# Kernel optimization log

Measured on AMD Instinct MI355X. Metric: run time of the kernel, lower is better.

The kernel has to match this reference:

```python
import jax, jax.numpy as jnp
import numpy as np

EPS_NORM = 1e-12   # torch F.normalize eps
EPS_COND = 1e-10   # conductance denominator eps (matches source)


def _metrics(rep, b):
    # rep: (N, D) float, b: (N,) int 0/1 boundaries
    N = rep.shape[0]
    S = rep @ rep.T                                   # (N, N) similarity
    # F.normalize(sim, p=2, dim=-1): L2-normalize each row
    S = S / jnp.maximum(jnp.linalg.norm(S, axis=-1, keepdims=True), EPS_NORM)
    comm = jnp.cumsum(b)                              # (N,) community ids in [0, N]
    total = S.sum()
    deg = S.sum(axis=1)                               # row sums
    # modularity: sum over same-community (i, j) of S_ij - deg_i*deg_j/total, then /total
    same = comm[:, None] == comm[None, :]
    mod = jnp.sum(jnp.where(same, S - deg[:, None] * deg[None, :] / total, 0.0)) / total
    # conductance via segment sums over community ids (num_segments fixed = N+1)
    C = N + 1
    A = jax.ops.segment_sum(S, comm, num_segments=C)          # (C, N): sum over rows i in comm c
    B2 = jax.ops.segment_sum(A.T, comm, num_segments=C)      # (C_j, C_i)
    within = jnp.diagonal(B2)                                 # within-community edge weight
    row_tot = A.sum(axis=1)                                   # total weight incident to comm c
    between = row_tot - within
    counts = jax.ops.segment_sum(jnp.ones((N,), dtype=S.dtype), comm, num_segments=C)
    nonempty = counts > 0
    cond_terms = jnp.where(nonempty, between / (2.0 * within + between + EPS_COND), 0.0)
    n_comms = jnp.maximum(nonempty.sum(), 1).astype(S.dtype)
    cond = cond_terms.sum() / n_comms
    return mod, cond


def setup_inputs() -> dict:
    key = jax.random.key(0)
    k1, k2 = jax.random.split(key)
    representations = jax.random.normal(k1, (8, 2048, 512), dtype=jnp.float32)
    boundaries = jax.random.randint(k2, (8, 2048), 0, 2, dtype=jnp.int32)
    return {"representations": representations, "boundaries": boundaries}


def reference(representations, boundaries):
    mod, cond = jax.vmap(_metrics)(representations, boundaries)
    # (2, B): row 0 = modularity per batch, row 1 = conductance per batch
    return jnp.stack([mod, cond], axis=0)
```

## Files before the change

kernel.cpp:

```cpp
#include <hip/hip_runtime.h>
#include <hip/hip_bf16.h>

constexpr int BATCH = 8;
constexpr int N = 2048;
constexpr int D = 512;

using short8 = __attribute__((ext_vector_type(8))) short;
using half8 = __attribute__((ext_vector_type(8))) _Float16;
using floatx4 = __attribute__((ext_vector_type(4))) float;

__global__ __launch_bounds__(256) void convert_kernel(const float* __restrict__ in,
                                                      unsigned short* __restrict__ hi,
                                                      unsigned short* __restrict__ lo) {
    size_t base = ((size_t)blockIdx.x * 256 + threadIdx.x) * 8;
    float v[8];
    *(float4*)(v) = *(const float4*)(in + base);
    *(float4*)(v + 4) = *(const float4*)(in + base + 4);
    short8 h, l;
#pragma unroll
    for (int e = 0; e < 8; ++e) {
        _Float16 hh = (_Float16)v[e];
        float r = v[e] - (float)hh;
        _Float16 ll = (_Float16)r;
        h[e] = __builtin_bit_cast(short, hh);
        l[e] = __builtin_bit_cast(short, ll);
    }
    *(short8*)(hi + base) = h;
    *(short8*)(lo + base) = l;
}

__global__ __launch_bounds__(256) void scan_kernel(const int* __restrict__ b,
                                                   int* __restrict__ comm,
                                                   float* __restrict__ stats ) {
    int batch = blockIdx.x;
    int t = threadIdx.x;

    {
        int idx = batch * 256 + t;
        float* p = stats;
#pragma unroll
        for (int u = 0; u < 24; ++u) p[idx + u * 2048] = 0.0f;
    }

    const int* bb = b + batch * N;
    int* cc = comm + batch * N;

    int vals[8];
    int s = 0;
#pragma unroll
    for (int u = 0; u < 8; ++u) { vals[u] = bb[t * 8 + u]; s += vals[u]; }

    __shared__ int ps[256];
    ps[t] = s;
    __syncthreads();
    for (int off = 1; off < 256; off <<= 1) {
        int v = (t >= off) ? ps[t - off] : 0;
        __syncthreads();
        ps[t] += v;
        __syncthreads();
    }
    int run = (t > 0) ? ps[t - 1] : 0;
#pragma unroll
    for (int u = 0; u < 8; ++u) { run += vals[u]; cc[t * 8 + u] = run; }
}

__global__ __launch_bounds__(256, 3) void gemm_mfma(
        const unsigned short* __restrict__ Hhi, const unsigned short* __restrict__ Hlo,
        const int* __restrict__ comm,
        float* __restrict__ ssq, float* __restrict__ sm, float* __restrict__ bs) {
    int batch = blockIdx.z;

    int t = blockIdx.x;
    int bi = 0;
    while (t >= (16 - bi)) { t -= (16 - bi); ++bi; }
    int bj = bi + t;
    bool diag = (bi == bj);
    int i0 = bi * 128, j0 = bj * 128;

    __shared__ unsigned short sAhi[4096], sAlo[4096], sBhi[4096], sBlo[4096];
    __shared__ int sci[128], scj[128];

    int tid = threadIdx.x;
    const int* cm = comm + batch * N;
    if (tid < 128) { sci[tid] = cm[i0 + tid]; scj[tid] = cm[j0 + tid]; }

    const size_t bo = (size_t)batch * N * D;
    int srow = tid >> 2;
    int kg = (tid & 3) ^ ((srow >> 1) & 3);
    size_t gA0 = bo + (size_t)(i0 + srow) * D + kg * 8;
    size_t gA1 = gA0 + (size_t)64 * D;
    size_t gB0 = bo + (size_t)(j0 + srow) * D + kg * 8;
    size_t gB1 = gB0 + (size_t)64 * D;

    int lane = tid & 63;
    int wv = tid >> 6;
    int wrow = wv >> 1, wcol = wv & 1;
    int l15 = lane & 15, lhi = lane >> 4;

    int offA[4], offB[4];
#pragma unroll
    for (int m = 0; m < 4; ++m) {
        int r = wrow * 64 + m * 16 + l15;
        offA[m] = r * 64 + ((lhi ^ ((r >> 1) & 3)) << 4);
        int c = wcol * 64 + m * 16 + l15;
        offB[m] = c * 64 + ((lhi ^ ((c >> 1) & 3)) << 4);
    }

    floatx4 acc[4][4];
#pragma unroll
    for (int m = 0; m < 4; ++m)
#pragma unroll
        for (int n = 0; n < 4; ++n) acc[m][n] = (floatx4){0.f, 0.f, 0.f, 0.f};

    int wbyte = tid * 16;

    short8 rAh0 = *(const short8*)(Hhi + gA0);
    short8 rAh1 = *(const short8*)(Hhi + gA1);
    short8 rAl0 = *(const short8*)(Hlo + gA0);
    short8 rAl1 = *(const short8*)(Hlo + gA1);
    short8 rBh0 = *(const short8*)(Hhi + gB0);
    short8 rBh1 = *(const short8*)(Hhi + gB1);
    short8 rBl0 = *(const short8*)(Hlo + gB0);
    short8 rBl1 = *(const short8*)(Hlo + gB1);

#pragma unroll 1
    for (int kt = 0; kt < 16; ++kt) {
        *(short8*)((char*)sAhi + wbyte) = rAh0;
        *(short8*)((char*)sAhi + wbyte + 4096) = rAh1;
        *(short8*)((char*)sAlo + wbyte) = rAl0;
        *(short8*)((char*)sAlo + wbyte + 4096) = rAl1;
        *(short8*)((char*)sBhi + wbyte) = rBh0;
        *(short8*)((char*)sBhi + wbyte + 4096) = rBh1;
        *(short8*)((char*)sBlo + wbyte) = rBl0;
        *(short8*)((char*)sBlo + wbyte + 4096) = rBl1;
        __syncthreads();

        if (kt < 15) {
            size_t k = (size_t)(kt + 1) * 32;
            rAh0 = *(const short8*)(Hhi + gA0 + k);
            rAh1 = *(const short8*)(Hhi + gA1 + k);
            rAl0 = *(const short8*)(Hlo + gA0 + k);
            rAl1 = *(const short8*)(Hlo + gA1 + k);
            rBh0 = *(const short8*)(Hhi + gB0 + k);
            rBh1 = *(const short8*)(Hhi + gB1 + k);
            rBl0 = *(const short8*)(Hlo + gB0 + k);
            rBl1 = *(const short8*)(Hlo + gB1 + k);
        }

        half8 ah[4], al[4], bh[4], bl[4];
#pragma unroll
        for (int m = 0; m < 4; ++m) {
            ah[m] = *(const half8*)((const char*)sAhi + offA[m]);
            al[m] = *(const half8*)((const char*)sAlo + offA[m]);
            bh[m] = *(const half8*)((const char*)sBhi + offB[m]);
            bl[m] = *(const half8*)((const char*)sBlo + offB[m]);
        }
#pragma unroll
        for (int m = 0; m < 4; ++m)
#pragma unroll
            for (int n = 0; n < 4; ++n) {
                acc[m][n] = __builtin_amdgcn_mfma_f32_16x16x32_f16(ah[m], bh[n], acc[m][n], 0, 0, 0);
                acc[m][n] = __builtin_amdgcn_mfma_f32_16x16x32_f16(ah[m], bl[n], acc[m][n], 0, 0, 0);
                acc[m][n] = __builtin_amdgcn_mfma_f32_16x16x32_f16(al[m], bh[n], acc[m][n], 0, 0, 0);
            }
        __syncthreads();
    }

    float* pssq = ssq + batch * N;
    float* psm = sm + batch * N;
    float* pbs = bs + batch * N;

    int cjv[4];
#pragma unroll
    for (int n = 0; n < 4; ++n) cjv[n] = scj[wcol * 64 + n * 16 + l15];

    float cq[4] = {0.f, 0.f, 0.f, 0.f};
    float cs[4] = {0.f, 0.f, 0.f, 0.f};
    float cb[4] = {0.f, 0.f, 0.f, 0.f};

#pragma unroll
    for (int m = 0; m < 4; ++m) {
#pragma unroll
        for (int rr = 0; rr < 4; ++rr) {
            int rloc = wrow * 64 + m * 16 + lhi * 4 + rr;
            int civ = sci[rloc];
            float vq = 0.f, vs = 0.f, vb = 0.f;
#pragma unroll
            for (int n = 0; n < 4; ++n) {
                float g = acc[m][n][rr];
                float gq = g * g;
                float gb = (civ == cjv[n]) ? g : 0.f;
                vq += gq; vs += g; vb += gb;
                cq[n] += gq; cs[n] += g; cb[n] += gb;
            }
#pragma unroll
            for (int msk = 8; msk >= 1; msk >>= 1) {
                vq += __shfl_xor(vq, msk);
                vs += __shfl_xor(vs, msk);
                vb += __shfl_xor(vb, msk);
            }
            if (l15 == 0) {
                atomicAdd(&pssq[i0 + rloc], vq);
                atomicAdd(&psm[i0 + rloc], vs);
                atomicAdd(&pbs[i0 + rloc], vb);
            }
        }
    }

    if (!diag) {
#pragma unroll
        for (int n = 0; n < 4; ++n) {
            cq[n] += __shfl_xor(cq[n], 16); cq[n] += __shfl_xor(cq[n], 32);
            cs[n] += __shfl_xor(cs[n], 16); cs[n] += __shfl_xor(cs[n], 32);
            cb[n] += __shfl_xor(cb[n], 16); cb[n] += __shfl_xor(cb[n], 32);
            if (lhi == 0) {
                int col = j0 + wcol * 64 + n * 16 + l15;
                atomicAdd(&pssq[col], cq[n]);
                atomicAdd(&psm[col], cs[n]);
                atomicAdd(&pbs[col], cb[n]);
            }
        }
    }
}

__global__ __launch_bounds__(1024) void finalize(const float* __restrict__ ssq,
                                                 const float* __restrict__ sm,
                                                 const float* __restrict__ bs,
                                                 const int* __restrict__ comm,
                                                 float* __restrict__ out) {
    int batch = blockIdx.x;
    const float* pssq = ssq + batch * N;
    const float* psm = sm + batch * N;
    const float* pbs = bs + batch * N;
    const int* pcomm = comm + batch * N;
    int tid = threadIdx.x;

    __shared__ float sWc[N + 1];
    __shared__ float sTc[N + 1];
    __shared__ int sCnt[N + 1];

    for (int c = tid; c < N + 1; c += 1024) { sWc[c] = 0.0f; sTc[c] = 0.0f; sCnt[c] = 0; }
    __syncthreads();

    float totalLocal = 0.0f;
    for (int i = tid; i < N; i += 1024) {
        float r = sqrtf(pssq[i]);
        r = fmaxf(r, 1e-12f);
        float deg = psm[i] / r;
        float bn = pbs[i] / r;
        int c = pcomm[i];
        atomicAdd(&sTc[c], deg);
        atomicAdd(&sWc[c], bn);
        atomicAdd(&sCnt[c], 1);
        totalLocal += deg;
    }
    __syncthreads();

    float sumW = 0.0f, sumT2 = 0.0f, condSum = 0.0f, ncomm = 0.0f;
    for (int c = tid; c < N + 1; c += 1024) {
        if (sCnt[c] > 0) {
            float W = sWc[c];
            float T = sTc[c];
            sumW += W;
            sumT2 += T * T;
            float between = T - W;
            condSum += between / (2.0f * W + between + 1e-10f);
            ncomm += 1.0f;
        }
    }

    float vals[5] = {totalLocal, sumW, sumT2, condSum, ncomm};
#pragma unroll
    for (int v = 0; v < 5; ++v)
#pragma unroll
        for (int m = 32; m >= 1; m >>= 1) vals[v] += __shfl_xor(vals[v], m);

    __shared__ float part[5][16];
    int wid = tid >> 6;
    if ((tid & 63) == 0) {
#pragma unroll
        for (int v = 0; v < 5; ++v) part[v][wid] = vals[v];
    }
    __syncthreads();

    if (tid == 0) {
        float red[5];
#pragma unroll
        for (int v = 0; v < 5; ++v) {
            float a = 0.f;
            for (int w = 0; w < 16; ++w) a += part[v][w];
            red[v] = a;
        }
        float total = red[0];
        float mod = (red[1] - red[2] / total) / total;
        float cond = red[3] / fmaxf(red[4], 1.0f);
        out[batch] = mod;
        out[BATCH + batch] = cond;
    }
}

extern "C" void kernel_launch(void* const* d_in, const int* in_sizes, int n_in,
                              void* d_out, int out_size, void* d_ws, size_t ws_size,
                              hipStream_t stream) {
    const float* rep = (const float*)d_in[0];
    const int* bnd = (const int*)d_in[1];
    float* out = (float*)d_out;

    float* ssq = (float*)d_ws;
    float* sm = ssq + BATCH * N;
    float* bs = sm + BATCH * N;
    int* comm = (int*)(bs + BATCH * N);
    unsigned short* Hhi = (unsigned short*)((char*)d_ws + 256 * 1024);
    unsigned short* Hlo = Hhi + (size_t)BATCH * N * D;

    convert_kernel<<<(BATCH * N * D) / (256 * 8), 256, 0, stream>>>(rep, Hhi, Hlo);
    scan_kernel<<<BATCH, 256, 0, stream>>>(bnd, comm, ssq);

    dim3 grid(136, 1, BATCH);
    gemm_mfma<<<grid, 256, 0, stream>>>(Hhi, Hlo, comm, ssq, sm, bs);

    finalize<<<BATCH, 1024, 0, stream>>>(ssq, sm, bs, comm, out);
}
```

Measured before the change: 168.2 us.

## Double-buffer GEMM tiles with direct global-to-LDS loads and fuse prep kernels

Merges the fp32-to-fp16 hi/lo split kernel and the boundary scan kernel into a single launch. In the GEMM, the register-staged global loads are replaced by global_load_lds into a double-buffered shared-memory tile, so the next K tile streams in while MFMAs run on the current one. This also drops one barrier per iteration and removes the occupancy hint from launch_bounds. The cost is twice the LDS per block, which may lower occupancy. Correctness relies on global_load_lds completing before the end-of-iteration barrier, which the code does not enforce with an explicit vmcnt wait.

```diff
diff --git a/kernel.cpp b/kernel.cpp
--- a/kernel.cpp
+++ b/kernel.cpp
@@ -9,42 +9,48 @@
 using half8 = __attribute__((ext_vector_type(8))) _Float16;
 using floatx4 = __attribute__((ext_vector_type(4))) float;
 
-__global__ __launch_bounds__(256) void convert_kernel(const float* __restrict__ in,
-                                                      unsigned short* __restrict__ hi,
-                                                      unsigned short* __restrict__ lo) {
-    size_t base = ((size_t)blockIdx.x * 256 + threadIdx.x) * 8;
-    float v[8];
-    *(float4*)(v) = *(const float4*)(in + base);
-    *(float4*)(v + 4) = *(const float4*)(in + base + 4);
-    short8 h, l;
-#pragma unroll
-    for (int e = 0; e < 8; ++e) {
-        _Float16 hh = (_Float16)v[e];
-        float r = v[e] - (float)hh;
-        _Float16 ll = (_Float16)r;
-        h[e] = __builtin_bit_cast(short, hh);
-        l[e] = __builtin_bit_cast(short, ll);
-    }
-    *(short8*)(hi + base) = h;
-    *(short8*)(lo + base) = l;
-}
-
-__global__ __launch_bounds__(256) void scan_kernel(const int* __restrict__ b,
+__device__ __forceinline__ void gload16(const void* g, void* l) {
+    __builtin_amdgcn_global_load_lds(
+        (const __attribute__((address_space(1))) unsigned int*)g,
+        (__attribute__((address_space(3))) unsigned int*)l, 16, 0, 0);
+}
+
+__global__ __launch_bounds__(256) void prep_kernel(const float* __restrict__ in,
+                                                   unsigned short* __restrict__ hi,
+                                                   unsigned short* __restrict__ lo,
+                                                   const int* __restrict__ b,
                                                    int* __restrict__ comm,
                                                    float* __restrict__ stats ) {
-    int batch = blockIdx.x;
+    int blk = blockIdx.x;
     int t = threadIdx.x;
-
+    if (blk < 4096) {
+        size_t base = ((size_t)blk * 256 + t) * 8;
+        float v[8];
+        *(float4*)(v) = *(const float4*)(in + base);
+        *(float4*)(v + 4) = *(const float4*)(in + base + 4);
+        short8 h, l;
+#pragma unroll
+        for (int e = 0; e < 8; ++e) {
+            _Float16 hh = (_Float16)v[e];
+            float r = v[e] - (float)hh;
+            _Float16 ll = (_Float16)r;
+            h[e] = __builtin_bit_cast(short, hh);
+            l[e] = __builtin_bit_cast(short, ll);
+        }
+        *(short8*)(hi + base) = h;
+        *(short8*)(lo + base) = l;
+        return;
+    }
+
+    int batch = blk - 4096;
     {
         int idx = batch * 256 + t;
-        float* p = stats;
-#pragma unroll
-        for (int u = 0; u < 24; ++u) p[idx + u * 2048] = 0.0f;
+#pragma unroll
+        for (int u = 0; u < 24; ++u) stats[idx + u * 2048] = 0.0f;
     }
 
     const int* bb = b + batch * N;
     int* cc = comm + batch * N;
-
     int vals[8];
     int s = 0;
 #pragma unroll
@@ -64,7 +70,7 @@
     for (int u = 0; u < 8; ++u) { run += vals[u]; cc[t * 8 + u] = run; }
 }
 
-__global__ __launch_bounds__(256, 3) void gemm_mfma(
+__global__ __launch_bounds__(256) void gemm_mfma(
         const unsigned short* __restrict__ Hhi, const unsigned short* __restrict__ Hlo,
         const int* __restrict__ comm,
         float* __restrict__ ssq, float* __restrict__ sm, float* __restrict__ bs) {
@@ -77,7 +83,7 @@
     bool diag = (bi == bj);
     int i0 = bi * 128, j0 = bj * 128;
 
-    __shared__ unsigned short sAhi[4096], sAlo[4096], sBhi[4096], sBlo[4096];
+    __shared__ unsigned short S[2][4][4096];
     __shared__ int sci[128], scj[128];
 
     int tid = threadIdx.x;
@@ -87,10 +93,14 @@
     const size_t bo = (size_t)batch * N * D;
     int srow = tid >> 2;
     int kg = (tid & 3) ^ ((srow >> 1) & 3);
-    size_t gA0 = bo + (size_t)(i0 + srow) * D + kg * 8;
-    size_t gA1 = gA0 + (size_t)64 * D;
-    size_t gB0 = bo + (size_t)(j0 + srow) * D + kg * 8;
-    size_t gB1 = gB0 + (size_t)64 * D;
+    const unsigned short* pAhi0 = Hhi + bo + (size_t)(i0 + srow) * D + kg * 8;
+    const unsigned short* pAhi1 = pAhi0 + (size_t)64 * D;
+    const unsigned short* pAlo0 = Hlo + bo + (size_t)(i0 + srow) * D + kg * 8;
+    const unsigned short* pAlo1 = pAlo0 + (size_t)64 * D;
+    const unsigned short* pBhi0 = Hhi + bo + (size_t)(j0 + srow) * D + kg * 8;
+    const unsigned short* pBhi1 = pBhi0 + (size_t)64 * D;
+    const unsigned short* pBlo0 = Hlo + bo + (size_t)(j0 + srow) * D + kg * 8;
+    const unsigned short* pBlo1 = pBlo0 + (size_t)64 * D;
 
     int lane = tid & 63;
     int wv = tid >> 6;
@@ -112,48 +122,37 @@
 #pragma unroll
         for (int n = 0; n < 4; ++n) acc[m][n] = (floatx4){0.f, 0.f, 0.f, 0.f};
 
-    int wbyte = tid * 16;
-
-    short8 rAh0 = *(const short8*)(Hhi + gA0);
-    short8 rAh1 = *(const short8*)(Hhi + gA1);
-    short8 rAl0 = *(const short8*)(Hlo + gA0);
-    short8 rAl1 = *(const short8*)(Hlo + gA1);
-    short8 rBh0 = *(const short8*)(Hhi + gB0);
-    short8 rBh1 = *(const short8*)(Hhi + gB1);
-    short8 rBl0 = *(const short8*)(Hlo + gB0);
-    short8 rBl1 = *(const short8*)(Hlo + gB1);
+#define ISSUE_TILE(B, KO)                                        \
+    do {                                                         \
+        gload16(pAhi0 + (KO), &S[B][0][tid * 8]);                \
+        gload16(pAhi1 + (KO), &S[B][0][2048 + tid * 8]);         \
+        gload16(pAlo0 + (KO), &S[B][1][tid * 8]);                \
+        gload16(pAlo1 + (KO), &S[B][1][2048 + tid * 8]);         \
+        gload16(pBhi0 + (KO), &S[B][2][tid * 8]);                \
+        gload16(pBhi1 + (KO), &S[B][2][2048 + tid * 8]);         \
+        gload16(pBlo0 + (KO), &S[B][3][tid * 8]);                \
+        gload16(pBlo1 + (KO), &S[B][3][2048 + tid * 8]);         \
+    } while (0)
+
+    ISSUE_TILE(0, 0);
+    __syncthreads();
 
 #pragma unroll 1
     for (int kt = 0; kt < 16; ++kt) {
-        *(short8*)((char*)sAhi + wbyte) = rAh0;
-        *(short8*)((char*)sAhi + wbyte + 4096) = rAh1;
-        *(short8*)((char*)sAlo + wbyte) = rAl0;
-        *(short8*)((char*)sAlo + wbyte + 4096) = rAl1;
-        *(short8*)((char*)sBhi + wbyte) = rBh0;
-        *(short8*)((char*)sBhi + wbyte + 4096) = rBh1;
-        *(short8*)((char*)sBlo + wbyte) = rBl0;
-        *(short8*)((char*)sBlo + wbyte + 4096) = rBl1;
-        __syncthreads();
-
+        int cur = kt & 1;
         if (kt < 15) {
-            size_t k = (size_t)(kt + 1) * 32;
-            rAh0 = *(const short8*)(Hhi + gA0 + k);
-            rAh1 = *(const short8*)(Hhi + gA1 + k);
-            rAl0 = *(const short8*)(Hlo + gA0 + k);
-            rAl1 = *(const short8*)(Hlo + gA1 + k);
-            rBh0 = *(const short8*)(Hhi + gB0 + k);
-            rBh1 = *(const short8*)(Hhi + gB1 + k);
-            rBl0 = *(const short8*)(Hlo + gB0 + k);
-            rBl1 = *(const short8*)(Hlo + gB1 + k);
-        }
-
+            int ko = (kt + 1) * 32;
+            ISSUE_TILE(cur ^ 1, ko);
+        }
+
+        const char* base = (const char*)&S[cur][0][0];
         half8 ah[4], al[4], bh[4], bl[4];
 #pragma unroll
         for (int m = 0; m < 4; ++m) {
-            ah[m] = *(const half8*)((const char*)sAhi + offA[m]);
-            al[m] = *(const half8*)((const char*)sAlo + offA[m]);
-            bh[m] = *(const half8*)((const char*)sBhi + offB[m]);
-            bl[m] = *(const half8*)((const char*)sBlo + offB[m]);
+            ah[m] = *(const half8*)(base + offA[m]);
+            al[m] = *(const half8*)(base + 8192 + offA[m]);
+            bh[m] = *(const half8*)(base + 16384 + offB[m]);
+            bl[m] = *(const half8*)(base + 24576 + offB[m]);
         }
 #pragma unroll
         for (int m = 0; m < 4; ++m)
@@ -165,6 +164,7 @@
             }
         __syncthreads();
     }
+#undef ISSUE_TILE
 
     float* pssq = ssq + batch * N;
     float* psm = sm + batch * N;
@@ -313,8 +313,7 @@
     unsigned short* Hhi = (unsigned short*)((char*)d_ws + 256 * 1024);
     unsigned short* Hlo = Hhi + (size_t)BATCH * N * D;
 
-    convert_kernel<<<(BATCH * N * D) / (256 * 8), 256, 0, stream>>>(rep, Hhi, Hlo);
-    scan_kernel<<<BATCH, 256, 0, stream>>>(bnd, comm, ssq);
+    prep_kernel<<<4096 + BATCH, 256, 0, stream>>>(rep, Hhi, Hlo, bnd, comm, ssq);
 
     dim3 grid(136, 1, BATCH);
     gemm_mfma<<<grid, 256, 0, stream>>>(Hhi, Hlo, comm, ssq, sm, bs);
```

Result: slower. 178.0 us (+5.8%).
